# Performance work log

Hardware: AMD Instinct MI355X
Metric: run time of the kernel (lower is better)

Reference implementation:

```python
import jax, jax.numpy as jnp
import numpy as np

SEQ, D, HID, C = 512, 768, 128, 5
NENT, SPAN = 128, 16


def setup_inputs() -> dict:
    key = jax.random.key(0)
    ks = jax.random.split(key, 24)
    s = 0.02

    def rn(k, shape, scale=s):
        return jax.random.normal(k, shape, dtype=jnp.float32) * scale

    inp = {
        "encoder_output": rn(ks[0], (1, SEQ, D), 1.0),
        "holder_idxs": jax.random.randint(ks[1], (NENT, SPAN), 0, SEQ, dtype=jnp.int32),
        "target_idxs": jax.random.randint(ks[2], (NENT, SPAN), 0, SEQ, dtype=jnp.int32),
        "exp_idxs": jax.random.randint(ks[3], (NENT, SPAN), 0, SEQ, dtype=jnp.int32),
    }
    names = ["Wh_f", "bh_f", "Wh_b", "bh_b", "Wt_f", "bt_f", "Wt_b", "bt_b",
             "We_f", "be_f", "We_b", "be_b"]
    for n, k in zip(names, ks[4:16]):
        shape = (4 * HID, D) if n.startswith("W") else (4 * HID,)
        inp[n] = rn(k, shape)
    inp["T_he"] = rn(ks[16], (2 * HID, 2 * HID, 2 * HID))
    inp["T_te"] = rn(ks[17], (2 * HID, 2 * HID, 2 * HID))
    inp["T_cls"] = rn(ks[18], (2 * HID, C, 2 * HID))
    return inp


def _lstm_cell_step(x, W_ih, b):
    # Single LSTM step with h0=c0=0 (the torch module feeds seq_len=1 to nn.LSTM,
    # so W_hh @ h0 vanishes; b = b_ih + b_hh). Gate order: i, f, g, o.
    g = x @ W_ih.T + b                         # [n, L, 4H]
    i, f, gg, o = jnp.split(g, 4, axis=-1)
    c = jax.nn.sigmoid(i) * jnp.tanh(gg)
    return jax.nn.sigmoid(o) * jnp.tanh(c)     # h, [n, L, H]


def _lstm_pool(enc_seq, idxs, Wf, bf, Wb, bb):
    toks = enc_seq[idxs]                       # [n, L, D] gather
    h = jnp.concatenate([_lstm_cell_step(toks, Wf, bf),
                         _lstm_cell_step(toks, Wb, bb)], axis=-1)  # [n, L, 2H]
    return h.max(axis=1)                       # max-pool over span -> [n, 2H]


def reference(encoder_output, holder_idxs, target_idxs, exp_idxs,
              Wh_f, bh_f, Wh_b, bh_b, Wt_f, bt_f, Wt_b, bt_b,
              We_f, be_f, We_b, be_b, T_he, T_te, T_cls):
    enc = encoder_output[0]                    # [SEQ, D]
    He = _lstm_pool(enc, holder_idxs, Wh_f, bh_f, Wh_b, bh_b)   # [nh, 2H]
    Te = _lstm_pool(enc, target_idxs, Wt_f, bt_f, Wt_b, bt_b)   # [nt, 2H]
    Ee = _lstm_pool(enc, exp_idxs, We_f, be_f, We_b, be_b)      # [ne, 2H]

    # hep[i,k] = He[i] @ T_he @ Ee[k];  tep[j,k] = Te[j] @ T_te @ Ee[k]
    hep = jnp.einsum('ia,abc,kc->ikb', He, T_he, Ee)            # [nh, ne, 2H]
    tep = jnp.einsum('ja,abc,kc->jkb', Te, T_te, Ee)            # [nt, ne, 2H]
    # pred[i,j,k,m] = tep[j,k] @ T_cls[:,m,:] @ hep[i,k]
    pred = jnp.einsum('jkb,bmc,ikc->ijkm', tep, T_cls, hep)     # [nh, nt, ne, C]
    return pred
```

## Files before the change

### kernel.cpp

```cpp
#include <hip/hip_runtime.h>
#include <hip/hip_bf16.h>
#include <math.h>

#define DIM   768
#define HID   128
#define H2    256
#define NENT  128
#define SPAN  16
#define NCLS  5

#define POOLB_OFF 0
#define HEPB_OFF  196608
#define TEPB_OFF  (HEPB_OFF + 8388608)
#define TCLSB_OFF (TEPB_OFF + 8388608)
#define WB_OFF    (TCLSB_OFF + 655360)
#define TOKB_OFF  21168128
#define GATES_OFF (TOKB_OFF + 9437184)
#define PREDT_OFF 21168128

typedef __attribute__((ext_vector_type(8))) short bf16x8;
typedef __attribute__((ext_vector_type(4))) float f32x4;

__device__ __forceinline__ float sigmoidf_(float x) { return 1.0f / (1.0f + __expf(-x)); }

__device__ __forceinline__ unsigned short f2bf(float x) {
    __hip_bfloat16 h = __float2bfloat16(x);
    return *reinterpret_cast<unsigned short*>(&h);
}

__global__ __launch_bounds__(256)
void prep_kernel(const float* __restrict__ Whf, const float* __restrict__ Whb,
                 const float* __restrict__ Wtf, const float* __restrict__ Wtb,
                 const float* __restrict__ Wef, const float* __restrict__ Web,
                 const float* __restrict__ Tcls, const float* __restrict__ enc,
                 const int* __restrict__ idx_h, const int* __restrict__ idx_t,
                 const int* __restrict__ idx_e,
                 unsigned short* __restrict__ WB, unsigned short* __restrict__ TB,
                 unsigned short* __restrict__ tokB)
{
    const int bb = blockIdx.x;
    const int tid = threadIdx.x;
    if (bb < 1728) {
        int gid = bb * 256 + tid;
        int t2  = gid / 73728;
        int rem = gid % 73728;
        int n   = rem / 192;
        int c4  = rem % 192;
        int gate = n >> 7, j = n & 127;
        int srow = (gate == 0) ? j : (gate == 1) ? 256 + j : 384 + j;
        const float* W = (t2 == 0) ? Whf : (t2 == 1) ? Whb : (t2 == 2) ? Wtf :
                         (t2 == 3) ? Wtb : (t2 == 4) ? Wef : Web;
        float4 v = ((const float4*)(W + srow * DIM))[c4];
        unsigned short* d = WB + ((size_t)(t2 * 384 + n)) * DIM + c4 * 4;
        d[0] = f2bf(v.x); d[1] = f2bf(v.y); d[2] = f2bf(v.z); d[3] = f2bf(v.w);
    } else if (bb < 3008) {
        int idx = (bb - 1728) * 256 + tid;
        int b = idx / (NCLS * H2);
        int r = idx % (NCLS * H2);
        int m = r >> 8, c = r & 255;
        TB[((m << 8) + c) * H2 + b] = f2bf(Tcls[idx]);
    } else {
        int gid = (bb - 3008) * 256 + tid;
        int r  = gid / 192, c4 = gid % 192;
        int type = r >> 11;
        int rem  = r & 2047;
        const int* idx = (type == 0) ? idx_h : (type == 1) ? idx_t : idx_e;
        int row = idx[rem];
        float4 v = ((const float4*)(enc + (size_t)row * DIM))[c4];
        unsigned short h4[4] = { f2bf(v.x), f2bf(v.y), f2bf(v.z), f2bf(v.w) };
        *(uint2*)(tokB + (size_t)r * DIM + c4 * 4) = *(uint2*)h4;
    }
}

__global__ __launch_bounds__(256)
void gates_mfma(const unsigned short* __restrict__ tokB,
                const unsigned short* __restrict__ WB,
                float* __restrict__ gates)
{
    __shared__ unsigned short As[2][128 * 64];
    __shared__ unsigned short Bs[2][128 * 64];
    const int lbid = ((int)blockIdx.x & 7) * 36 + ((int)blockIdx.x >> 3);
    const int type = lbid / 96;
    const int rem  = lbid % 96;
    const int mb0  = (rem / 6) * 128;
    const int nb0  = (rem % 6) * 128;
    const int tid = threadIdx.x;
    const int w = tid >> 6, l = tid & 63;
    const int lr = l & 15, lg = l >> 4;
    const unsigned short* A = tokB + (size_t)type * 2048 * DIM + (size_t)mb0 * DIM;
    const unsigned short* B = WB   + (size_t)type * 768  * DIM + (size_t)nb0 * DIM;

    const int sr0 = tid >> 3;
    const int sc  = tid & 7;

    bf16x8 ra[4], rb[4];
    #define LOADT(kt)                                                        \
        {                                                                    \
            const int koff = (kt) * 64 + sc * 8;                             \
            _Pragma("unroll")                                                \
            for (int p = 0; p < 4; ++p) {                                    \
                int rr = sr0 + p * 32;                                       \
                ra[p] = *(const bf16x8*)(A + (size_t)rr * DIM + koff);       \
                rb[p] = *(const bf16x8*)(B + (size_t)rr * DIM + koff);       \
            }                                                                \
        }
    #define WRITET(buf)                                                      \
        {                                                                    \
            _Pragma("unroll")                                                \
            for (int p = 0; p < 4; ++p) {                                    \
                int rr = sr0 + p * 32;                                       \
                int bo = (rr * 128 + sc * 16) ^ ((rr & 7) << 4);             \
                *(bf16x8*)((char*)As[buf] + bo) = ra[p];                     \
                *(bf16x8*)((char*)Bs[buf] + bo) = rb[p];                     \
            }                                                                \
        }

    f32x4 acc[4][4];
    #pragma unroll
    for (int mt = 0; mt < 4; ++mt)
        #pragma unroll
        for (int nt = 0; nt < 4; ++nt) acc[mt][nt] = (f32x4){0.f, 0.f, 0.f, 0.f};

    const int am0 = (w & 1) * 64;
    const int bn0 = (w >> 1) * 64;

    LOADT(0);
    WRITET(0);
    __syncthreads();

    int cur = 0;
    #pragma unroll 1
    for (int kt = 0; kt < 12; ++kt) {
        if (kt + 1 < 12) LOADT(kt + 1);

        #pragma unroll
        for (int ks = 0; ks < 2; ++ks) {
            bf16x8 af[4], bf[4];
            #pragma unroll
            for (int mt = 0; mt < 4; ++mt) {
                int rr = am0 + mt * 16 + lr;
                int bo = (rr * 128 + ks * 64 + lg * 16) ^ ((rr & 7) << 4);
                af[mt] = *(const bf16x8*)((const char*)As[cur] + bo);
            }
            #pragma unroll
            for (int nt = 0; nt < 4; ++nt) {
                int rr = bn0 + nt * 16 + lr;
                int bo = (rr * 128 + ks * 64 + lg * 16) ^ ((rr & 7) << 4);
                bf[nt] = *(const bf16x8*)((const char*)Bs[cur] + bo);
            }
            #pragma unroll
            for (int mt = 0; mt < 4; ++mt)
                #pragma unroll
                for (int nt = 0; nt < 4; ++nt)
                    acc[mt][nt] = __builtin_amdgcn_mfma_f32_16x16x32_bf16(af[mt], bf[nt], acc[mt][nt], 0, 0, 0);
        }

        if (kt + 1 < 12) {
            WRITET(cur ^ 1);
        }
        __syncthreads();
        cur ^= 1;
    }
    #undef LOADT
    #undef WRITET

    float* C = gates + (size_t)type * 2048 * 768 + (size_t)mb0 * 768 + nb0;
    #pragma unroll
    for (int mt = 0; mt < 4; ++mt)
        #pragma unroll
        for (int nt = 0; nt < 4; ++nt)
            #pragma unroll
            for (int r = 0; r < 4; ++r)
                C[(size_t)(am0 + mt * 16 + lg * 4 + r) * 768 + bn0 + nt * 16 + lr] = acc[mt][nt][r];
}

__global__ __launch_bounds__(256)
void pool_epilogue(const float* __restrict__ gates,
                   const float* __restrict__ bhf, const float* __restrict__ bhb,
                   const float* __restrict__ btf, const float* __restrict__ btb,
                   const float* __restrict__ bef, const float* __restrict__ beb,
                   unsigned short* __restrict__ poolB)
{
    const int type = blockIdx.x >> 7;
    const int ent  = blockIdx.x & 127;
    const int tid  = threadIdx.x;
    const int dir  = tid >> 7;
    const int j    = tid & 127;
    const float* Bv = (type == 0) ? (dir ? bhb : bhf)
                    : (type == 1) ? (dir ? btb : btf)
                                  : (dir ? beb : bef);
    const float bi = Bv[j], bg = Bv[2 * HID + j], bo = Bv[3 * HID + j];
    const float* g0 = gates + ((size_t)type * 2048 + ent * 16) * 768 + dir * 384 + j;
    float hmax = -1e30f;
    #pragma unroll
    for (int l = 0; l < SPAN; ++l) {
        const float* gr = g0 + l * 768;
        float iv = sigmoidf_(gr[0]   + bi);
        float gv = tanhf(   gr[128] + bg);
        float ov = sigmoidf_(gr[256] + bo);
        hmax = fmaxf(hmax, ov * tanhf(iv * gv));
    }
    poolB[(size_t)(type * NENT + ent) * H2 + dir * HID + j] = f2bf(hmax);
}

__global__ __launch_bounds__(1024)
void pair_mfma(const unsigned short* __restrict__ EeB,
               const unsigned short* __restrict__ HeB,
               const unsigned short* __restrict__ TeB,
               const float* __restrict__ T0, const float* __restrict__ T1,
               unsigned short* __restrict__ hepN,
               unsigned short* __restrict__ tepN)
{
    __shared__ __align__(16) char smem[131072];
    const int bid = blockIdx.x;
    const int t = bid >> 8;
    const int b = bid & 255;
    const float* T = t ? T1 : T0;
    const unsigned short* Hx = t ? TeB : HeB;
    unsigned short* outp = t ? tepN : hepN;
    const int tid = threadIdx.x;
    const int w = tid >> 6, l = tid & 63;
    const int lr = l & 15, lg = l >> 4;

    {
        const int r0 = tid >> 5;
        const int ch = tid & 31;
        #pragma unroll
        for (int p = 0; p < 8; ++p) {
            int row = p * 32 + r0;
            const float* src = T + ((size_t)row * 256 + b) * 256 + ch * 8;
            float4 v0 = ((const float4*)src)[0];
            float4 v1 = ((const float4*)src)[1];
            bf16x8 hv; unsigned short* hp = (unsigned short*)&hv;
            hp[0]=f2bf(v0.x); hp[1]=f2bf(v0.y); hp[2]=f2bf(v0.z); hp[3]=f2bf(v0.w);
            hp[4]=f2bf(v1.x); hp[5]=f2bf(v1.y); hp[6]=f2bf(v1.z); hp[7]=f2bf(v1.w);
            int bo = (row * 512 + ch * 16) ^ ((row & 7) << 4);
            *(bf16x8*)(smem + bo) = hv;
        }
    }
    __syncthreads();

    f32x4 acc1[4][2];
    {
        const int aw = (w & 3) * 64;
        const int kw = (w >> 2) * 32;
        #pragma unroll
        for (int mt = 0; mt < 4; ++mt)
            #pragma unroll
            for (int nt = 0; nt < 2; ++nt) acc1[mt][nt] = (f32x4){0.f, 0.f, 0.f, 0.f};

        #pragma unroll
        for (int ks = 0; ks < 8; ++ks) {
            bf16x8 af[4], bf[2];
            #pragma unroll
            for (int mt = 0; mt < 4; ++mt) {
                int ar = aw + mt * 16 + lr;
                int bo = (ar * 512 + (ks * 32 + lg * 8) * 2) ^ ((ar & 7) << 4);
                af[mt] = *(const bf16x8*)(smem + bo);
            }
            #pragma unroll
            for (int nt = 0; nt < 2; ++nt)
                bf[nt] = *(const bf16x8*)(EeB + (kw + nt * 16 + lr) * H2 + ks * 32 + lg * 8);
            #pragma unroll
            for (int mt = 0; mt < 4; ++mt)
                #pragma unroll
                for (int nt = 0; nt < 2; ++nt)
                    acc1[mt][nt] = __builtin_amdgcn_mfma_f32_16x16x32_bf16(af[mt], bf[nt], acc1[mt][nt], 0, 0, 0);
        }
    }
    __syncthreads();

    {
        const int aw = (w & 3) * 64;
        const int kw = (w >> 2) * 32;
        #pragma unroll
        for (int mt = 0; mt < 4; ++mt)
            #pragma unroll
            for (int nt = 0; nt < 2; ++nt) {
                int k  = kw + nt * 16 + lr;
                int a0 = aw + mt * 16 + lg * 4;
                unsigned short h4[4] = { f2bf(acc1[mt][nt][0]), f2bf(acc1[mt][nt][1]),
                                         f2bf(acc1[mt][nt][2]), f2bf(acc1[mt][nt][3]) };
                int bo = (k * 512 + a0 * 2) ^ ((k & 7) << 4);
                *(uint2*)(smem + bo) = *(uint2*)h4;
            }
    }
    __syncthreads();

    {
        const int kw2 = (w >> 3) * 64;
        const int iw  = (w & 7) * 16;
        f32x4 acc2[4];
        #pragma unroll
        for (int mt = 0; mt < 4; ++mt) acc2[mt] = (f32x4){0.f, 0.f, 0.f, 0.f};

        #pragma unroll
        for (int ks = 0; ks < 8; ++ks) {
            bf16x8 af[4], bf;
            #pragma unroll
            for (int mt = 0; mt < 4; ++mt) {
                int kr = kw2 + mt * 16 + lr;
                int bo = (kr * 512 + (ks * 32 + lg * 8) * 2) ^ ((kr & 7) << 4);
                af[mt] = *(const bf16x8*)(smem + bo);
            }
            bf = *(const bf16x8*)(Hx + (iw + lr) * H2 + ks * 32 + lg * 8);
            #pragma unroll
            for (int mt = 0; mt < 4; ++mt)
                acc2[mt] = __builtin_amdgcn_mfma_f32_16x16x32_bf16(af[mt], bf, acc2[mt], 0, 0, 0);
        }
        unsigned short* po = outp + (size_t)b * (128 * 128);
        #pragma unroll
        for (int mt = 0; mt < 4; ++mt)
            #pragma unroll
            for (int r = 0; r < 4; ++r) {
                int k = kw2 + mt * 16 + lg * 4 + r;
                int i = iw + lr;
                po[k * 128 + i] = f2bf(acc2[mt][r]);
            }
    }
}

__global__ __launch_bounds__(512)
void step3_mfma(const unsigned short* __restrict__ hepN,
                const unsigned short* __restrict__ tepN,
                const unsigned short* __restrict__ TclsB,
                float* __restrict__ predT)
{
    __shared__ unsigned short hepS[128 * 256];
    __shared__ unsigned short tepS[64 * 256];
    __shared__ unsigned short WS[64 * 256];
    const int lbid = (blockIdx.x & 7) * 32 + (blockIdx.x >> 3);
    const int k  = lbid >> 1;
    const int jh = lbid & 1;
    const int tid = threadIdx.x;
    const int w  = tid >> 6;
    const int l  = tid & 63;
    const int lr = l & 15;
    const int lg = l >> 4;
    const int swz = (lr & 7) << 4;

    #pragma unroll
    for (int q = 0; q < 4; ++q) {
        int bcol = q * 64 + l;
        bf16x8 v = *(const bf16x8*)(tepN + ((size_t)bcol * 128 + k) * 128 + jh * 64 + w * 8);
        #pragma unroll
        for (int r = 0; r < 8; ++r) {
            int j = w * 8 + r;
            int bo = (j * 512 + bcol * 2) ^ (r << 4);
            *(unsigned short*)((char*)tepS + bo) = ((unsigned short*)&v)[r];
        }
    }
    #pragma unroll
    for (int s = 0; s < 2; ++s)
        #pragma unroll
        for (int q = 0; q < 4; ++q) {
            int bcol = q * 64 + l;
            bf16x8 v = *(const bf16x8*)(hepN + ((size_t)bcol * 128 + k) * 128 + w * 16 + s * 8);
            #pragma unroll
            for (int r = 0; r < 8; ++r) {
                int i = w * 16 + s * 8 + r;
                int bo = (i * 512 + bcol * 2) ^ (r << 4);
                *(unsigned short*)((char*)hepS + bo) = ((unsigned short*)&v)[r];
            }
        }
    __syncthreads();

    bf16x8 ha[8];
    #pragma unroll
    for (int ks = 0; ks < 8; ++ks) {
        int ir = w * 16 + lr;
        int bo = (ir * 512 + (ks * 32 + lg * 8) * 2) ^ ((ir & 7) << 4);
        ha[ks] = *(const bf16x8*)((const char*)hepS + bo);
    }

    #pragma unroll 1
    for (int m = 0; m < NCLS; ++m) {
        {
            const unsigned short* tcm = TclsB + (size_t)m * (H2 * H2);
            f32x4 acc1[4][2];
            #pragma unroll
            for (int jt = 0; jt < 4; ++jt)
                #pragma unroll
                for (int ct = 0; ct < 2; ++ct) acc1[jt][ct] = (f32x4){0.f, 0.f, 0.f, 0.f};

            #pragma unroll
            for (int ks = 0; ks < 8; ++ks) {
                bf16x8 a[4], bb[2];
                #pragma unroll
                for (int jt = 0; jt < 4; ++jt) {
                    int byteoff = ((((jt * 16 + lr) << 8) + ks * 32 + lg * 8) << 1) ^ swz;
                    a[jt] = *(const bf16x8*)((const char*)tepS + byteoff);
                }
                #pragma unroll
                for (int ct = 0; ct < 2; ++ct)
                    bb[ct] = *(const bf16x8*)(tcm + (size_t)(w * 32 + ct * 16 + lr) * H2 + ks * 32 + lg * 8);
                #pragma unroll
                for (int jt = 0; jt < 4; ++jt)
                    #pragma unroll
                    for (int ct = 0; ct < 2; ++ct)
                        acc1[jt][ct] = __builtin_amdgcn_mfma_f32_16x16x32_bf16(a[jt], bb[ct], acc1[jt][ct], 0, 0, 0);
            }
            #pragma unroll
            for (int jt = 0; jt < 4; ++jt)
                #pragma unroll
                for (int ct = 0; ct < 2; ++ct)
                    #pragma unroll
                    for (int r = 0; r < 4; ++r) {
                        int j = jt * 16 + lg * 4 + r;
                        int c = w * 32 + ct * 16 + lr;
                        int byteoff = ((((j << 8) + c)) << 1) ^ ((j & 7) << 4);
                        *(unsigned short*)((char*)WS + byteoff) = f2bf(acc1[jt][ct][r]);
                    }
        }
        __syncthreads();

        {
            f32x4 acc2[4];
            #pragma unroll
            for (int jt = 0; jt < 4; ++jt) acc2[jt] = (f32x4){0.f, 0.f, 0.f, 0.f};

            #pragma unroll
            for (int ks = 0; ks < 8; ++ks) {
                #pragma unroll
                for (int jt = 0; jt < 4; ++jt) {
                    int byteoff = ((((jt * 16 + lr) << 8) + ks * 32 + lg * 8) << 1) ^ swz;
                    bf16x8 wb = *(const bf16x8*)((const char*)WS + byteoff);
                    acc2[jt] = __builtin_amdgcn_mfma_f32_16x16x32_bf16(ha[ks], wb, acc2[jt], 0, 0, 0);
                }
            }
            float* po = predT + (size_t)(k * NCLS + m) * (NENT * NENT);
            #pragma unroll
            for (int jt = 0; jt < 4; ++jt)
                #pragma unroll
                for (int r = 0; r < 4; ++r) {
                    int i = w * 16 + lg * 4 + r;
                    int j = jh * 64 + jt * 16 + lr;
                    po[i * NENT + j] = acc2[jt][r];
                }
        }
        __syncthreads();
    }
}

__global__ __launch_bounds__(256)
void transpose_out(const float* __restrict__ predT, float* __restrict__ out)
{
    __shared__ float Ls[160][33];
    const int bid = blockIdx.x;
    const int ij0 = (bid >> 2) * 32;
    const int km0 = (bid & 3) * 160;
    const int t = threadIdx.x;

    #pragma unroll
    for (int q = 0; q < 20; ++q) {
        int r = (t >> 5) + q * 8;
        int c = t & 31;
        Ls[r][c] = predT[(size_t)(km0 + r) * 16384 + ij0 + c];
    }
    __syncthreads();
    for (int idx = t; idx < 32 * 160; idx += 256) {
        int r = idx / 160, c = idx % 160;
        out[(size_t)(ij0 + r) * 640 + km0 + c] = Ls[c][r];
    }
}

extern "C" void kernel_launch(void* const* d_in, const int* in_sizes, int n_in,
                              void* d_out, int out_size, void* d_ws, size_t ws_size,
                              hipStream_t stream)
{
    (void)in_sizes; (void)n_in; (void)out_size; (void)ws_size;
    const float* enc  = (const float*)d_in[0];
    const int*   hidx = (const int*)d_in[1];
    const int*   tidx = (const int*)d_in[2];
    const int*   eidx = (const int*)d_in[3];
    const float* Whf = (const float*)d_in[4];
    const float* bhf = (const float*)d_in[5];
    const float* Whb = (const float*)d_in[6];
    const float* bhb = (const float*)d_in[7];
    const float* Wtf = (const float*)d_in[8];
    const float* btf = (const float*)d_in[9];
    const float* Wtb = (const float*)d_in[10];
    const float* btb = (const float*)d_in[11];
    const float* Wef = (const float*)d_in[12];
    const float* bef = (const float*)d_in[13];
    const float* Web = (const float*)d_in[14];
    const float* beb = (const float*)d_in[15];
    const float* T_he  = (const float*)d_in[16];
    const float* T_te  = (const float*)d_in[17];
    const float* T_cls = (const float*)d_in[18];

    float* out = (float*)d_out;
    char*  ws  = (char*)d_ws;
    unsigned short* poolB = (unsigned short*)(ws + POOLB_OFF);
    unsigned short* hepN  = (unsigned short*)(ws + HEPB_OFF);
    unsigned short* tepN  = (unsigned short*)(ws + TEPB_OFF);
    unsigned short* TclsB = (unsigned short*)(ws + TCLSB_OFF);
    unsigned short* WB    = (unsigned short*)(ws + WB_OFF);
    unsigned short* tokB  = (unsigned short*)(ws + TOKB_OFF);
    float*          gates = (float*)(ws + GATES_OFF);
    float*          predT = (float*)(ws + PREDT_OFF);

    unsigned short* HeB = poolB;
    unsigned short* TeB = poolB + 1 * NENT * H2;
    unsigned short* EeB = poolB + 2 * NENT * H2;

    prep_kernel<<<7616, 256, 0, stream>>>(Whf, Whb, Wtf, Wtb, Wef, Web,
                                          T_cls, enc, hidx, tidx, eidx,
                                          WB, TclsB, tokB);

    gates_mfma<<<288, 256, 0, stream>>>(tokB, WB, gates);

    pool_epilogue<<<384, 256, 0, stream>>>(gates, bhf, bhb, btf, btb, bef, beb, poolB);

    pair_mfma<<<512, 1024, 0, stream>>>(EeB, HeB, TeB, T_he, T_te, hepN, tepN);

    step3_mfma<<<256, 512, 0, stream>>>(hepN, tepN, TclsB, predT);

    transpose_out<<<2048, 256, 0, stream>>>(predT, out);
}
```

Before: 134.8 us.

## Split pair bilinear into two GEMM kernels with contiguous T_he/T_te reads

Replaces the fused per-b pair kernel with two kernels. The first reads each T[a] slice contiguously and computes T[a]·Ee^T into a bf16 global intermediate laid out [b][a][k]. The second transposes each b-slice in LDS and multiplies by He/Te to produce hep/tep. This removes the strided gather over T but adds a large global round-trip for the intermediate, scalar LDS transpose stores, and an extra launch.

```diff
diff --git a/kernel.cpp b/kernel.cpp
--- a/kernel.cpp
+++ b/kernel.cpp
@@ -16,6 +16,8 @@
 #define WB_OFF    (TCLSB_OFF + 655360)
 #define TOKB_OFF  21168128
 #define GATES_OFF (TOKB_OFF + 9437184)
+#define TMP30_OFF 21168128
+#define TMP31_OFF (TMP30_OFF + 16777216)
 #define PREDT_OFF 21168128
 
 typedef __attribute__((ext_vector_type(8))) short bf16x8;
@@ -204,20 +206,16 @@
 }
 
 __global__ __launch_bounds__(1024)
-void pair_mfma(const unsigned short* __restrict__ EeB,
-               const unsigned short* __restrict__ HeB,
-               const unsigned short* __restrict__ TeB,
-               const float* __restrict__ T0, const float* __restrict__ T1,
-               unsigned short* __restrict__ hepN,
-               unsigned short* __restrict__ tepN)
+void gemm1_mfma(const unsigned short* __restrict__ EeB,
+                const float* __restrict__ T0, const float* __restrict__ T1,
+                unsigned short* __restrict__ tmp30, unsigned short* __restrict__ tmp31)
 {
     __shared__ __align__(16) char smem[131072];
     const int bid = blockIdx.x;
     const int t = bid >> 8;
-    const int b = bid & 255;
+    const int a = bid & 255;
     const float* T = t ? T1 : T0;
-    const unsigned short* Hx = t ? TeB : HeB;
-    unsigned short* outp = t ? tepN : hepN;
+    unsigned short* outp = t ? tmp31 : tmp30;
     const int tid = threadIdx.x;
     const int w = tid >> 6, l = tid & 63;
     const int lr = l & 15, lg = l >> 4;
@@ -225,10 +223,11 @@
     {
         const int r0 = tid >> 5;
         const int ch = tid & 31;
+        const float* base = T + (size_t)a * 65536;
         #pragma unroll
         for (int p = 0; p < 8; ++p) {
             int row = p * 32 + r0;
-            const float* src = T + ((size_t)row * 256 + b) * 256 + ch * 8;
+            const float* src = base + row * 256 + ch * 8;
             float4 v0 = ((const float4*)src)[0];
             float4 v1 = ((const float4*)src)[1];
             bf16x8 hv; unsigned short* hp = (unsigned short*)&hv;
@@ -240,84 +239,114 @@
     }
     __syncthreads();
 
-    f32x4 acc1[4][2];
+    const int bw = (w & 7) * 32;
+    const int kw = (w >> 3) * 64;
+    f32x4 acc[2][4];
+    #pragma unroll
+    for (int mt = 0; mt < 2; ++mt)
+        #pragma unroll
+        for (int nt = 0; nt < 4; ++nt) acc[mt][nt] = (f32x4){0.f, 0.f, 0.f, 0.f};
+
+    #pragma unroll
+    for (int ks = 0; ks < 8; ++ks) {
+        bf16x8 af[2], bf[4];
+        #pragma unroll
+        for (int mt = 0; mt < 2; ++mt) {
+            int br = bw + mt * 16 + lr;
+            int bo = (br * 512 + (ks * 32 + lg * 8) * 2) ^ ((br & 7) << 4);
+            af[mt] = *(const bf16x8*)(smem + bo);
+        }
+        #pragma unroll
+        for (int nt = 0; nt < 4; ++nt)
+            bf[nt] = *(const bf16x8*)(EeB + (kw + nt * 16 + lr) * H2 + ks * 32 + lg * 8);
+        #pragma unroll
+        for (int mt = 0; mt < 2; ++mt)
+            #pragma unroll
+            for (int nt = 0; nt < 4; ++nt)
+                acc[mt][nt] = __builtin_amdgcn_mfma_f32_16x16x32_bf16(af[mt], bf[nt], acc[mt][nt], 0, 0, 0);
+    }
+
+    #pragma unroll
+    for (int mt = 0; mt < 2; ++mt)
+        #pragma unroll
+        for (int nt = 0; nt < 4; ++nt)
+            #pragma unroll
+            for (int r = 0; r < 4; ++r) {
+                int b_ = bw + mt * 16 + lg * 4 + r;
+                int k_ = kw + nt * 16 + lr;
+                outp[((size_t)b_ * 256 + a) * 128 + k_] = f2bf(acc[mt][nt][r]);
+            }
+}
+
+__global__ __launch_bounds__(512)
+void gemm2_mfma(const unsigned short* __restrict__ HeB, const unsigned short* __restrict__ TeB,
+                const unsigned short* __restrict__ tmp30, const unsigned short* __restrict__ tmp31,
+                unsigned short* __restrict__ hepN, unsigned short* __restrict__ tepN)
+{
+    __shared__ unsigned short WT[128 * 256];
+    const int bid = blockIdx.x;
+    const int t = bid >> 8;
+    const int b = bid & 255;
+    const unsigned short* src = (t ? tmp31 : tmp30) + (size_t)b * 32768;
+    const unsigned short* Hx = t ? TeB : HeB;
+    unsigned short* outp = (t ? tepN : hepN) + (size_t)b * 16384;
+    const int tid = threadIdx.x;
+    const int w = tid >> 6, l = tid & 63;
+    const int lr = l & 15, lg = l >> 4;
+
     {
-        const int aw = (w & 3) * 64;
-        const int kw = (w >> 2) * 32;
+        const int a0 = tid >> 4;
+        const int k8 = (tid & 15) * 8;
+        #pragma unroll
+        for (int it = 0; it < 8; ++it) {
+            int aa = it * 32 + a0;
+            bf16x8 v = *(const bf16x8*)(src + aa * 128 + k8);
+            #pragma unroll
+            for (int j = 0; j < 8; ++j) {
+                int kk = k8 + j;
+                int bo = (kk * 512 + aa * 2) ^ (j << 4);
+                *(unsigned short*)((char*)WT + bo) = ((unsigned short*)&v)[j];
+            }
+        }
+    }
+    __syncthreads();
+
+    const int kw = (w & 1) * 64;
+    const int iw = (w >> 1) * 32;
+    f32x4 acc[4][2];
+    #pragma unroll
+    for (int mt = 0; mt < 4; ++mt)
+        #pragma unroll
+        for (int nt = 0; nt < 2; ++nt) acc[mt][nt] = (f32x4){0.f, 0.f, 0.f, 0.f};
+
+    #pragma unroll
+    for (int ks = 0; ks < 8; ++ks) {
+        bf16x8 af[4], bf[2];
+        #pragma unroll
+        for (int mt = 0; mt < 4; ++mt) {
+            int kr = kw + mt * 16 + lr;
+            int bo = (kr * 512 + (ks * 32 + lg * 8) * 2) ^ ((kr & 7) << 4);
+            af[mt] = *(const bf16x8*)((const char*)WT + bo);
+        }
+        #pragma unroll
+        for (int nt = 0; nt < 2; ++nt)
+            bf[nt] = *(const bf16x8*)(Hx + (iw + nt * 16 + lr) * H2 + ks * 32 + lg * 8);
         #pragma unroll
         for (int mt = 0; mt < 4; ++mt)
             #pragma unroll
-            for (int nt = 0; nt < 2; ++nt) acc1[mt][nt] = (f32x4){0.f, 0.f, 0.f, 0.f};
-
-        #pragma unroll
-        for (int ks = 0; ks < 8; ++ks) {
-            bf16x8 af[4], bf[2];
-            #pragma unroll
-            for (int mt = 0; mt < 4; ++mt) {
-                int ar = aw + mt * 16 + lr;
-                int bo = (ar * 512 + (ks * 32 + lg * 8) * 2) ^ ((ar & 7) << 4);
-                af[mt] = *(const bf16x8*)(smem + bo);
-            }
-            #pragma unroll
             for (int nt = 0; nt < 2; ++nt)
-                bf[nt] = *(const bf16x8*)(EeB + (kw + nt * 16 + lr) * H2 + ks * 32 + lg * 8);
-            #pragma unroll
-            for (int mt = 0; mt < 4; ++mt)
-                #pragma unroll
-                for (int nt = 0; nt < 2; ++nt)
-                    acc1[mt][nt] = __builtin_amdgcn_mfma_f32_16x16x32_bf16(af[mt], bf[nt], acc1[mt][nt], 0, 0, 0);
-        }
-    }
-    __syncthreads();
-
-    {
-        const int aw = (w & 3) * 64;
-        const int kw = (w >> 2) * 32;
-        #pragma unroll
-        for (int mt = 0; mt < 4; ++mt)
-            #pragma unroll
-            for (int nt = 0; nt < 2; ++nt) {
-                int k  = kw + nt * 16 + lr;
-                int a0 = aw + mt * 16 + lg * 4;
-                unsigned short h4[4] = { f2bf(acc1[mt][nt][0]), f2bf(acc1[mt][nt][1]),
-                                         f2bf(acc1[mt][nt][2]), f2bf(acc1[mt][nt][3]) };
-                int bo = (k * 512 + a0 * 2) ^ ((k & 7) << 4);
-                *(uint2*)(smem + bo) = *(uint2*)h4;
-            }
-    }
-    __syncthreads();
-
-    {
-        const int kw2 = (w >> 3) * 64;
-        const int iw  = (w & 7) * 16;
-        f32x4 acc2[4];
-        #pragma unroll
-        for (int mt = 0; mt < 4; ++mt) acc2[mt] = (f32x4){0.f, 0.f, 0.f, 0.f};
-
-        #pragma unroll
-        for (int ks = 0; ks < 8; ++ks) {
-            bf16x8 af[4], bf;
-            #pragma unroll
-            for (int mt = 0; mt < 4; ++mt) {
-                int kr = kw2 + mt * 16 + lr;
-                int bo = (kr * 512 + (ks * 32 + lg * 8) * 2) ^ ((kr & 7) << 4);
-                af[mt] = *(const bf16x8*)(smem + bo);
-            }
-            bf = *(const bf16x8*)(Hx + (iw + lr) * H2 + ks * 32 + lg * 8);
-            #pragma unroll
-            for (int mt = 0; mt < 4; ++mt)
-                acc2[mt] = __builtin_amdgcn_mfma_f32_16x16x32_bf16(af[mt], bf, acc2[mt], 0, 0, 0);
-        }
-        unsigned short* po = outp + (size_t)b * (128 * 128);
-        #pragma unroll
-        for (int mt = 0; mt < 4; ++mt)
+                acc[mt][nt] = __builtin_amdgcn_mfma_f32_16x16x32_bf16(af[mt], bf[nt], acc[mt][nt], 0, 0, 0);
+    }
+    #pragma unroll
+    for (int mt = 0; mt < 4; ++mt)
+        #pragma unroll
+        for (int nt = 0; nt < 2; ++nt)
             #pragma unroll
             for (int r = 0; r < 4; ++r) {
-                int k = kw2 + mt * 16 + lg * 4 + r;
-                int i = iw + lr;
-                po[k * 128 + i] = f2bf(acc2[mt][r]);
-            }
-    }
+                int k_ = kw + mt * 16 + lg * 4 + r;
+                int i_ = iw + nt * 16 + lr;
+                outp[k_ * 128 + i_] = f2bf(acc[mt][nt][r]);
+            }
 }
 
 __global__ __launch_bounds__(512)
@@ -498,6 +527,8 @@
     unsigned short* WB    = (unsigned short*)(ws + WB_OFF);
     unsigned short* tokB  = (unsigned short*)(ws + TOKB_OFF);
     float*          gates = (float*)(ws + GATES_OFF);
+    unsigned short* tmp30 = (unsigned short*)(ws + TMP30_OFF);
+    unsigned short* tmp31 = (unsigned short*)(ws + TMP31_OFF);
     float*          predT = (float*)(ws + PREDT_OFF);
 
     unsigned short* HeB = poolB;
@@ -512,7 +543,9 @@
 
     pool_epilogue<<<384, 256, 0, stream>>>(gates, bhf, bhb, btf, btb, bef, beb, poolB);
 
-    pair_mfma<<<512, 1024, 0, stream>>>(EeB, HeB, TeB, T_he, T_te, hepN, tepN);
+    gemm1_mfma<<<512, 1024, 0, stream>>>(EeB, T_he, T_te, tmp30, tmp31);
+
+    gemm2_mfma<<<512, 512, 0, stream>>>(HeB, TeB, tmp30, tmp31, hepN, tepN);
 
     step3_mfma<<<256, 512, 0, stream>>>(hepN, tepN, TclsB, predT);
 
```

Measured after the change: 168.5 us. 25.0% more time.

## Store gates as bf16 and pre-transpose T_he to bf16 in the pooling kernel

Applied to the files above, without the earlier changes.

The gates GEMM now writes bf16 instead of fp32, which halves gate write and read traffic. The pool epilogue kernel gains extra blocks that convert T_he to bf16 in a b-major layout, so the pair kernel's t=0 blocks read contiguous bf16 slabs instead of strided fp32 rows. The shared-memory layout in the pair kernel is reorganised into 128-byte-row banks with a new swizzle. The trade-offs are lower gate precision, since values are rounded to bf16 before the activations, and extra workspace writes for the transposed T_he.

```diff
diff --git a/kernel.cpp b/kernel.cpp
--- a/kernel.cpp
+++ b/kernel.cpp
@@ -9,14 +9,15 @@
 #define SPAN  16
 #define NCLS  5
 
-#define POOLB_OFF 0
-#define HEPB_OFF  196608
-#define TEPB_OFF  (HEPB_OFF + 8388608)
-#define TCLSB_OFF (TEPB_OFF + 8388608)
-#define WB_OFF    (TCLSB_OFF + 655360)
-#define TOKB_OFF  21168128
-#define GATES_OFF (TOKB_OFF + 9437184)
-#define PREDT_OFF 21168128
+#define POOLB_OFF  0
+#define HEPB_OFF   196608
+#define TEPB_OFF   (HEPB_OFF + 8388608)
+#define TCLSB_OFF  (TEPB_OFF + 8388608)
+#define WB_OFF     (TCLSB_OFF + 655360)
+#define TOKB_OFF   21168128
+#define TB_OFF     21168128
+#define GATESB_OFF 58060800
+#define PREDT_OFF  21168128
 
 typedef __attribute__((ext_vector_type(8))) short bf16x8;
 typedef __attribute__((ext_vector_type(4))) float f32x4;
@@ -26,6 +27,10 @@
 __device__ __forceinline__ unsigned short f2bf(float x) {
     __hip_bfloat16 h = __float2bfloat16(x);
     return *reinterpret_cast<unsigned short*>(&h);
+}
+__device__ __forceinline__ float bf2f(unsigned short u) {
+    unsigned int v = ((unsigned int)u) << 16;
+    float f; __builtin_memcpy(&f, &v, 4); return f;
 }
 
 __global__ __launch_bounds__(256)
@@ -75,7 +80,7 @@
 __global__ __launch_bounds__(256)
 void gates_mfma(const unsigned short* __restrict__ tokB,
                 const unsigned short* __restrict__ WB,
-                float* __restrict__ gates)
+                unsigned short* __restrict__ gatesB)
 {
     __shared__ unsigned short As[2][128 * 64];
     __shared__ unsigned short Bs[2][128 * 64];
@@ -164,127 +169,151 @@
     #undef LOADT
     #undef WRITET
 
-    float* C = gates + (size_t)type * 2048 * 768 + (size_t)mb0 * 768 + nb0;
+    unsigned short* C = gatesB + (size_t)type * 2048 * 768 + (size_t)mb0 * 768 + nb0;
     #pragma unroll
     for (int mt = 0; mt < 4; ++mt)
         #pragma unroll
         for (int nt = 0; nt < 4; ++nt)
             #pragma unroll
             for (int r = 0; r < 4; ++r)
-                C[(size_t)(am0 + mt * 16 + lg * 4 + r) * 768 + bn0 + nt * 16 + lr] = acc[mt][nt][r];
+                C[(size_t)(am0 + mt * 16 + lg * 4 + r) * 768 + bn0 + nt * 16 + lr] = f2bf(acc[mt][nt][r]);
 }
 
 __global__ __launch_bounds__(256)
-void pool_epilogue(const float* __restrict__ gates,
-                   const float* __restrict__ bhf, const float* __restrict__ bhb,
-                   const float* __restrict__ btf, const float* __restrict__ btb,
-                   const float* __restrict__ bef, const float* __restrict__ beb,
-                   unsigned short* __restrict__ poolB)
-{
-    const int type = blockIdx.x >> 7;
-    const int ent  = blockIdx.x & 127;
-    const int tid  = threadIdx.x;
-    const int dir  = tid >> 7;
-    const int j    = tid & 127;
-    const float* Bv = (type == 0) ? (dir ? bhb : bhf)
-                    : (type == 1) ? (dir ? btb : btf)
-                                  : (dir ? beb : bef);
-    const float bi = Bv[j], bg = Bv[2 * HID + j], bo = Bv[3 * HID + j];
-    const float* g0 = gates + ((size_t)type * 2048 + ent * 16) * 768 + dir * 384 + j;
-    float hmax = -1e30f;
-    #pragma unroll
-    for (int l = 0; l < SPAN; ++l) {
-        const float* gr = g0 + l * 768;
-        float iv = sigmoidf_(gr[0]   + bi);
-        float gv = tanhf(   gr[128] + bg);
-        float ov = sigmoidf_(gr[256] + bo);
-        hmax = fmaxf(hmax, ov * tanhf(iv * gv));
-    }
-    poolB[(size_t)(type * NENT + ent) * H2 + dir * HID + j] = f2bf(hmax);
+void poolconv(const unsigned short* __restrict__ gatesB,
+              const float* __restrict__ bhf, const float* __restrict__ bhb,
+              const float* __restrict__ btf, const float* __restrict__ btb,
+              const float* __restrict__ bef, const float* __restrict__ beb,
+              unsigned short* __restrict__ poolB,
+              const float* __restrict__ T0, unsigned short* __restrict__ TB)
+{
+    const int bb = blockIdx.x;
+    const int tid = threadIdx.x;
+    if (bb < 384) {
+        const int type = bb >> 7;
+        const int ent  = bb & 127;
+        const int dir  = tid >> 7;
+        const int j    = tid & 127;
+        const float* Bv = (type == 0) ? (dir ? bhb : bhf)
+                        : (type == 1) ? (dir ? btb : btf)
+                                      : (dir ? beb : bef);
+        const float bi = Bv[j], bg = Bv[2 * HID + j], bo = Bv[3 * HID + j];
+        const unsigned short* g0 = gatesB + ((size_t)type * 2048 + ent * 16) * 768 + dir * 384 + j;
+        float hmax = -1e30f;
+        #pragma unroll
+        for (int ll = 0; ll < SPAN; ++ll) {
+            const unsigned short* gr = g0 + ll * 768;
+            float iv = sigmoidf_(bf2f(gr[0])   + bi);
+            float gv = tanhf(   bf2f(gr[128]) + bg);
+            float ov = sigmoidf_(bf2f(gr[256]) + bo);
+            hmax = fmaxf(hmax, ov * tanhf(iv * gv));
+        }
+        poolB[(size_t)(type * NENT + ent) * H2 + dir * HID + j] = f2bf(hmax);
+    } else {
+        int W0 = (bb - 384) * 256 + tid;
+        #pragma unroll 1
+        for (int it = 0; it < 16; ++it) {
+            int idx = W0 + it * 131072;
+            int a  = idx >> 13;
+            int rr = idx & 8191;
+            int b  = rr >> 5;
+            int c8 = rr & 31;
+            const float* src = T0 + ((size_t)(a * 256 + b) << 8) + c8 * 8;
+            float4 v0 = ((const float4*)src)[0];
+            float4 v1 = ((const float4*)src)[1];
+            bf16x8 hv; unsigned short* hp = (unsigned short*)&hv;
+            hp[0]=f2bf(v0.x); hp[1]=f2bf(v0.y); hp[2]=f2bf(v0.z); hp[3]=f2bf(v0.w);
+            hp[4]=f2bf(v1.x); hp[5]=f2bf(v1.y); hp[6]=f2bf(v1.z); hp[7]=f2bf(v1.w);
+            *(bf16x8*)(TB + (((size_t)(b * 256 + a)) << 8) + c8 * 8) = hv;
+        }
+    }
 }
 
 __global__ __launch_bounds__(1024)
-void pair_mfma(const unsigned short* __restrict__ EeB,
-               const unsigned short* __restrict__ HeB,
-               const unsigned short* __restrict__ TeB,
-               const float* __restrict__ T0, const float* __restrict__ T1,
-               unsigned short* __restrict__ hepN,
-               unsigned short* __restrict__ tepN)
+void pairc_mfma(const unsigned short* __restrict__ EeB,
+                const unsigned short* __restrict__ HeB,
+                const unsigned short* __restrict__ TeB,
+                const unsigned short* __restrict__ TB,
+                const float* __restrict__ T1,
+                unsigned short* __restrict__ hepN, unsigned short* __restrict__ tepN)
 {
     __shared__ __align__(16) char smem[131072];
     const int bid = blockIdx.x;
     const int t = bid >> 8;
     const int b = bid & 255;
-    const float* T = t ? T1 : T0;
     const unsigned short* Hx = t ? TeB : HeB;
     unsigned short* outp = t ? tepN : hepN;
     const int tid = threadIdx.x;
     const int w = tid >> 6, l = tid & 63;
     const int lr = l & 15, lg = l >> 4;
 
-    {
-        const int r0 = tid >> 5;
-        const int ch = tid & 31;
+    if (t == 0) {
+        const unsigned short* TBb = TB + (size_t)b * 65536;
         #pragma unroll
         for (int p = 0; p < 8; ++p) {
-            int row = p * 32 + r0;
-            const float* src = T + ((size_t)row * 256 + b) * 256 + ch * 8;
+            int L = tid + p * 1024;
+            int row = L >> 5, ch = L & 31;
+            bf16x8 v = *(const bf16x8*)(TBb + (size_t)L * 8);
+            int bo = (((ch >> 3) << 15) + row * 128 + ((ch & 7) << 4)) ^ ((row & 7) << 4);
+            *(bf16x8*)(smem + bo) = v;
+        }
+    } else {
+        #pragma unroll
+        for (int p = 0; p < 8; ++p) {
+            int L = tid + p * 1024;
+            int row = L >> 5, ch = L & 31;
+            const float* src = T1 + ((size_t)row * 256 + b) * 256 + ch * 8;
             float4 v0 = ((const float4*)src)[0];
             float4 v1 = ((const float4*)src)[1];
             bf16x8 hv; unsigned short* hp = (unsigned short*)&hv;
             hp[0]=f2bf(v0.x); hp[1]=f2bf(v0.y); hp[2]=f2bf(v0.z); hp[3]=f2bf(v0.w);
             hp[4]=f2bf(v1.x); hp[5]=f2bf(v1.y); hp[6]=f2bf(v1.z); hp[7]=f2bf(v1.w);
-            int bo = (row * 512 + ch * 16) ^ ((row & 7) << 4);
+            int bo = (((ch >> 3) << 15) + row * 128 + ((ch & 7) << 4)) ^ ((row & 7) << 4);
             *(bf16x8*)(smem + bo) = hv;
         }
     }
     __syncthreads();
 
     f32x4 acc1[4][2];
-    {
-        const int aw = (w & 3) * 64;
-        const int kw = (w >> 2) * 32;
+    const int aw = (w & 3) * 64;
+    const int kw = (w >> 2) * 32;
+    #pragma unroll
+    for (int mt = 0; mt < 4; ++mt)
+        #pragma unroll
+        for (int nt = 0; nt < 2; ++nt) acc1[mt][nt] = (f32x4){0.f, 0.f, 0.f, 0.f};
+
+    #pragma unroll
+    for (int ks = 0; ks < 8; ++ks) {
+        const int cb = ks * 64 + lg * 16;
+        bf16x8 af[4], bf[2];
+        #pragma unroll
+        for (int mt = 0; mt < 4; ++mt) {
+            int a = aw + mt * 16 + lr;
+            int bo = (((cb >> 7) << 15) + a * 128 + (cb & 127)) ^ ((a & 7) << 4);
+            af[mt] = *(const bf16x8*)(smem + bo);
+        }
+        #pragma unroll
+        for (int nt = 0; nt < 2; ++nt)
+            bf[nt] = *(const bf16x8*)(EeB + (kw + nt * 16 + lr) * H2 + ks * 32 + lg * 8);
         #pragma unroll
         for (int mt = 0; mt < 4; ++mt)
             #pragma unroll
-            for (int nt = 0; nt < 2; ++nt) acc1[mt][nt] = (f32x4){0.f, 0.f, 0.f, 0.f};
-
-        #pragma unroll
-        for (int ks = 0; ks < 8; ++ks) {
-            bf16x8 af[4], bf[2];
-            #pragma unroll
-            for (int mt = 0; mt < 4; ++mt) {
-                int ar = aw + mt * 16 + lr;
-                int bo = (ar * 512 + (ks * 32 + lg * 8) * 2) ^ ((ar & 7) << 4);
-                af[mt] = *(const bf16x8*)(smem + bo);
-            }
-            #pragma unroll
             for (int nt = 0; nt < 2; ++nt)
-                bf[nt] = *(const bf16x8*)(EeB + (kw + nt * 16 + lr) * H2 + ks * 32 + lg * 8);
-            #pragma unroll
-            for (int mt = 0; mt < 4; ++mt)
-                #pragma unroll
-                for (int nt = 0; nt < 2; ++nt)
-                    acc1[mt][nt] = __builtin_amdgcn_mfma_f32_16x16x32_bf16(af[mt], bf[nt], acc1[mt][nt], 0, 0, 0);
-        }
+                acc1[mt][nt] = __builtin_amdgcn_mfma_f32_16x16x32_bf16(af[mt], bf[nt], acc1[mt][nt], 0, 0, 0);
     }
     __syncthreads();
 
-    {
-        const int aw = (w & 3) * 64;
-        const int kw = (w >> 2) * 32;
-        #pragma unroll
-        for (int mt = 0; mt < 4; ++mt)
-            #pragma unroll
-            for (int nt = 0; nt < 2; ++nt) {
-                int k  = kw + nt * 16 + lr;
-                int a0 = aw + mt * 16 + lg * 4;
-                unsigned short h4[4] = { f2bf(acc1[mt][nt][0]), f2bf(acc1[mt][nt][1]),
-                                         f2bf(acc1[mt][nt][2]), f2bf(acc1[mt][nt][3]) };
-                int bo = (k * 512 + a0 * 2) ^ ((k & 7) << 4);
-                *(uint2*)(smem + bo) = *(uint2*)h4;
-            }
-    }
+    #pragma unroll
+    for (int mt = 0; mt < 4; ++mt)
+        #pragma unroll
+        for (int nt = 0; nt < 2; ++nt) {
+            int k  = kw + nt * 16 + lr;
+            int a0 = aw + mt * 16 + lg * 4;
+            unsigned short h4[4] = { f2bf(acc1[mt][nt][0]), f2bf(acc1[mt][nt][1]),
+                                     f2bf(acc1[mt][nt][2]), f2bf(acc1[mt][nt][3]) };
+            int bo = (((a0 >> 6) << 14) + k * 128 + ((a0 & 63) << 1)) ^ ((k & 7) << 4);
+            *(uint2*)(smem + bo) = *(uint2*)h4;
+        }
     __syncthreads();
 
     {
@@ -296,11 +325,12 @@
 
         #pragma unroll
         for (int ks = 0; ks < 8; ++ks) {
+            const int ab = ks * 64 + lg * 16;
             bf16x8 af[4], bf;
             #pragma unroll
             for (int mt = 0; mt < 4; ++mt) {
-                int kr = kw2 + mt * 16 + lr;
-                int bo = (kr * 512 + (ks * 32 + lg * 8) * 2) ^ ((kr & 7) << 4);
+                int k = kw2 + mt * 16 + lr;
+                int bo = (((ab >> 7) << 14) + k * 128 + (ab & 127)) ^ ((k & 7) << 4);
                 af[mt] = *(const bf16x8*)(smem + bo);
             }
             bf = *(const bf16x8*)(Hx + (iw + lr) * H2 + ks * 32 + lg * 8);
@@ -491,14 +521,15 @@
 
     float* out = (float*)d_out;
     char*  ws  = (char*)d_ws;
-    unsigned short* poolB = (unsigned short*)(ws + POOLB_OFF);
-    unsigned short* hepN  = (unsigned short*)(ws + HEPB_OFF);
-    unsigned short* tepN  = (unsigned short*)(ws + TEPB_OFF);
-    unsigned short* TclsB = (unsigned short*)(ws + TCLSB_OFF);
-    unsigned short* WB    = (unsigned short*)(ws + WB_OFF);
-    unsigned short* tokB  = (unsigned short*)(ws + TOKB_OFF);
-    float*          gates = (float*)(ws + GATES_OFF);
-    float*          predT = (float*)(ws + PREDT_OFF);
+    unsigned short* poolB  = (unsigned short*)(ws + POOLB_OFF);
+    unsigned short* hepN   = (unsigned short*)(ws + HEPB_OFF);
+    unsigned short* tepN   = (unsigned short*)(ws + TEPB_OFF);
+    unsigned short* TclsB  = (unsigned short*)(ws + TCLSB_OFF);
+    unsigned short* WB     = (unsigned short*)(ws + WB_OFF);
+    unsigned short* tokB   = (unsigned short*)(ws + TOKB_OFF);
+    unsigned short* TB     = (unsigned short*)(ws + TB_OFF);
+    unsigned short* gatesB = (unsigned short*)(ws + GATESB_OFF);
+    float*          predT  = (float*)(ws + PREDT_OFF);
 
     unsigned short* HeB = poolB;
     unsigned short* TeB = poolB + 1 * NENT * H2;
@@ -508,11 +539,12 @@
                                           T_cls, enc, hidx, tidx, eidx,
                                           WB, TclsB, tokB);
 
-    gates_mfma<<<288, 256, 0, stream>>>(tokB, WB, gates);
-
-    pool_epilogue<<<384, 256, 0, stream>>>(gates, bhf, bhb, btf, btb, bef, beb, poolB);
-
-    pair_mfma<<<512, 1024, 0, stream>>>(EeB, HeB, TeB, T_he, T_te, hepN, tepN);
+    gates_mfma<<<288, 256, 0, stream>>>(tokB, WB, gatesB);
+
+    poolconv<<<896, 256, 0, stream>>>(gatesB, bhf, bhb, btf, btb, bef, beb,
+                                      poolB, T_he, TB);
+
+    pairc_mfma<<<512, 1024, 0, stream>>>(EeB, HeB, TeB, TB, T_te, hepN, tepN);
 
     step3_mfma<<<256, 512, 0, stream>>>(hepN, tepN, TclsB, predT);
 
```

New measurement: 140.9 us. 1.04x slower.

## Store gates in bf16, pre-transpose hep/tep, split step3 into finer blocks

Applied to the files above, without the earlier changes.

The gates GEMM now writes bf16 instead of fp32, which halves the gates traffic between gates_mfma and pool_epilogue. A new transpose kernel rewrites hep/tep into a k-major layout so step3 can load contiguous rows instead of doing a scattered transposing gather. step3 is split into 512 blocks, each covering 32 j values, to use more CUs with smaller LDS. This adds one kernel launch and an extra round trip through memory for the transpose, rounds the gate pre-activations to bf16, and makes each block recompute the hep fragments.

```diff
diff --git a/kernel.cpp b/kernel.cpp
--- a/kernel.cpp
+++ b/kernel.cpp
@@ -9,14 +9,16 @@
 #define SPAN  16
 #define NCLS  5
 
-#define POOLB_OFF 0
-#define HEPB_OFF  196608
-#define TEPB_OFF  (HEPB_OFF + 8388608)
-#define TCLSB_OFF (TEPB_OFF + 8388608)
-#define WB_OFF    (TCLSB_OFF + 655360)
-#define TOKB_OFF  21168128
-#define GATES_OFF (TOKB_OFF + 9437184)
-#define PREDT_OFF 21168128
+#define POOLB_OFF  0
+#define TCLSB_OFF  196608
+#define HEPT_OFF   851968
+#define TEPT_OFF   9240576
+#define HEPN_OFF   17629184
+#define TEPN_OFF   26017792
+#define GATESB_OFF 17629184
+#define PREDT_OFF  17629184
+#define WB_OFF     59572224
+#define TOKB_OFF   63111168
 
 typedef __attribute__((ext_vector_type(8))) short bf16x8;
 typedef __attribute__((ext_vector_type(4))) float f32x4;
@@ -26,6 +28,10 @@
 __device__ __forceinline__ unsigned short f2bf(float x) {
     __hip_bfloat16 h = __float2bfloat16(x);
     return *reinterpret_cast<unsigned short*>(&h);
+}
+__device__ __forceinline__ float bf2f(unsigned short u) {
+    unsigned int v = ((unsigned int)u) << 16;
+    float f; __builtin_memcpy(&f, &v, 4); return f;
 }
 
 __global__ __launch_bounds__(256)
@@ -75,7 +81,7 @@
 __global__ __launch_bounds__(256)
 void gates_mfma(const unsigned short* __restrict__ tokB,
                 const unsigned short* __restrict__ WB,
-                float* __restrict__ gates)
+                unsigned short* __restrict__ gatesB)
 {
     __shared__ unsigned short As[2][128 * 64];
     __shared__ unsigned short Bs[2][128 * 64];
@@ -164,18 +170,18 @@
     #undef LOADT
     #undef WRITET
 
-    float* C = gates + (size_t)type * 2048 * 768 + (size_t)mb0 * 768 + nb0;
+    unsigned short* C = gatesB + (size_t)type * 2048 * 768 + (size_t)mb0 * 768 + nb0;
     #pragma unroll
     for (int mt = 0; mt < 4; ++mt)
         #pragma unroll
         for (int nt = 0; nt < 4; ++nt)
             #pragma unroll
             for (int r = 0; r < 4; ++r)
-                C[(size_t)(am0 + mt * 16 + lg * 4 + r) * 768 + bn0 + nt * 16 + lr] = acc[mt][nt][r];
+                C[(size_t)(am0 + mt * 16 + lg * 4 + r) * 768 + bn0 + nt * 16 + lr] = f2bf(acc[mt][nt][r]);
 }
 
 __global__ __launch_bounds__(256)
-void pool_epilogue(const float* __restrict__ gates,
+void pool_epilogue(const unsigned short* __restrict__ gatesB,
                    const float* __restrict__ bhf, const float* __restrict__ bhb,
                    const float* __restrict__ btf, const float* __restrict__ btb,
                    const float* __restrict__ bef, const float* __restrict__ beb,
@@ -190,14 +196,14 @@
                     : (type == 1) ? (dir ? btb : btf)
                                   : (dir ? beb : bef);
     const float bi = Bv[j], bg = Bv[2 * HID + j], bo = Bv[3 * HID + j];
-    const float* g0 = gates + ((size_t)type * 2048 + ent * 16) * 768 + dir * 384 + j;
+    const unsigned short* g0 = gatesB + ((size_t)type * 2048 + ent * 16) * 768 + dir * 384 + j;
     float hmax = -1e30f;
     #pragma unroll
-    for (int l = 0; l < SPAN; ++l) {
-        const float* gr = g0 + l * 768;
-        float iv = sigmoidf_(gr[0]   + bi);
-        float gv = tanhf(   gr[128] + bg);
-        float ov = sigmoidf_(gr[256] + bo);
+    for (int ll = 0; ll < SPAN; ++ll) {
+        const unsigned short* gr = g0 + ll * 768;
+        float iv = sigmoidf_(bf2f(gr[0])   + bi);
+        float gv = tanhf(   bf2f(gr[128]) + bg);
+        float ov = sigmoidf_(bf2f(gr[256]) + bo);
         hmax = fmaxf(hmax, ov * tanhf(iv * gv));
     }
     poolB[(size_t)(type * NENT + ent) * H2 + dir * HID + j] = f2bf(hmax);
@@ -320,122 +326,135 @@
     }
 }
 
+__global__ __launch_bounds__(256)
+void trT(const unsigned short* __restrict__ hepN, const unsigned short* __restrict__ tepN,
+         unsigned short* __restrict__ hepT, unsigned short* __restrict__ tepT)
+{
+    __shared__ unsigned short L[128 * 256];
+    const int t = blockIdx.x >> 7;
+    const int k = blockIdx.x & 127;
+    const unsigned short* src = t ? tepN : hepN;
+    unsigned short* dst = (t ? tepT : hepT) + (size_t)k * 32768;
+    const int tid = threadIdx.x;
+
+    #pragma unroll
+    for (int it = 0; it < 16; ++it) {
+        int g = it * 256 + tid;
+        int b = g >> 4, i8 = g & 15;
+        bf16x8 v = *(const bf16x8*)(src + (size_t)b * 16384 + k * 128 + i8 * 8);
+        #pragma unroll
+        for (int e = 0; e < 8; ++e) {
+            int i = i8 * 8 + e;
+            int bo = (i * 512 + b * 2) ^ ((i8 & 7) << 4);
+            *(unsigned short*)((char*)L + bo) = ((unsigned short*)&v)[e];
+        }
+    }
+    __syncthreads();
+
+    #pragma unroll
+    for (int it = 0; it < 16; ++it) {
+        int h = it * 256 + tid;
+        int i = h >> 5, ch = h & 31;
+        int bo = (i * 512 + ch * 16) ^ (((i >> 3) & 7) << 4);
+        bf16x8 v = *(const bf16x8*)((const char*)L + bo);
+        *(bf16x8*)(dst + i * 256 + ch * 8) = v;
+    }
+}
+
 __global__ __launch_bounds__(512)
-void step3_mfma(const unsigned short* __restrict__ hepN,
-                const unsigned short* __restrict__ tepN,
-                const unsigned short* __restrict__ TclsB,
-                float* __restrict__ predT)
-{
-    __shared__ unsigned short hepS[128 * 256];
-    __shared__ unsigned short tepS[64 * 256];
-    __shared__ unsigned short WS[64 * 256];
-    const int lbid = (blockIdx.x & 7) * 32 + (blockIdx.x >> 3);
-    const int k  = lbid >> 1;
-    const int jh = lbid & 1;
+void step3v2(const unsigned short* __restrict__ hepT,
+             const unsigned short* __restrict__ tepT,
+             const unsigned short* __restrict__ TclsB,
+             float* __restrict__ predT)
+{
+    __shared__ unsigned short tepS[32 * 256];
+    __shared__ unsigned short WS[32 * 256];
+    const int lbid = ((int)blockIdx.x & 7) * 64 + ((int)blockIdx.x >> 3);
+    const int k  = lbid >> 2;
+    const int jq = lbid & 3;
+    const int j0 = jq * 32;
     const int tid = threadIdx.x;
-    const int w  = tid >> 6;
-    const int l  = tid & 63;
-    const int lr = l & 15;
-    const int lg = l >> 4;
-    const int swz = (lr & 7) << 4;
-
-    #pragma unroll
-    for (int q = 0; q < 4; ++q) {
-        int bcol = q * 64 + l;
-        bf16x8 v = *(const bf16x8*)(tepN + ((size_t)bcol * 128 + k) * 128 + jh * 64 + w * 8);
-        #pragma unroll
-        for (int r = 0; r < 8; ++r) {
-            int j = w * 8 + r;
-            int bo = (j * 512 + bcol * 2) ^ (r << 4);
-            *(unsigned short*)((char*)tepS + bo) = ((unsigned short*)&v)[r];
-        }
-    }
-    #pragma unroll
-    for (int s = 0; s < 2; ++s)
-        #pragma unroll
-        for (int q = 0; q < 4; ++q) {
-            int bcol = q * 64 + l;
-            bf16x8 v = *(const bf16x8*)(hepN + ((size_t)bcol * 128 + k) * 128 + w * 16 + s * 8);
-            #pragma unroll
-            for (int r = 0; r < 8; ++r) {
-                int i = w * 16 + s * 8 + r;
-                int bo = (i * 512 + bcol * 2) ^ (r << 4);
-                *(unsigned short*)((char*)hepS + bo) = ((unsigned short*)&v)[r];
-            }
-        }
-    __syncthreads();
+    const int w = tid >> 6, l = tid & 63;
+    const int lr = l & 15, lg = l >> 4;
+
+    #pragma unroll
+    for (int it = 0; it < 2; ++it) {
+        int g = it * 512 + tid;
+        int row = g >> 5, ch = g & 31;
+        bf16x8 v = *(const bf16x8*)(tepT + ((size_t)k * 128 + j0 + row) * 256 + ch * 8);
+        int bo = (row * 512 + ch * 16) ^ ((row & 7) << 4);
+        *(bf16x8*)((char*)tepS + bo) = v;
+    }
 
     bf16x8 ha[8];
     #pragma unroll
-    for (int ks = 0; ks < 8; ++ks) {
-        int ir = w * 16 + lr;
-        int bo = (ir * 512 + (ks * 32 + lg * 8) * 2) ^ ((ir & 7) << 4);
-        ha[ks] = *(const bf16x8*)((const char*)hepS + bo);
-    }
+    for (int ks = 0; ks < 8; ++ks)
+        ha[ks] = *(const bf16x8*)(hepT + ((size_t)k * 128 + w * 16 + lr) * 256 + ks * 32 + lg * 8);
+    __syncthreads();
 
     #pragma unroll 1
     for (int m = 0; m < NCLS; ++m) {
         {
             const unsigned short* tcm = TclsB + (size_t)m * (H2 * H2);
-            f32x4 acc1[4][2];
-            #pragma unroll
-            for (int jt = 0; jt < 4; ++jt)
-                #pragma unroll
-                for (int ct = 0; ct < 2; ++ct) acc1[jt][ct] = (f32x4){0.f, 0.f, 0.f, 0.f};
+            f32x4 a1[2][2];
+            #pragma unroll
+            for (int jt = 0; jt < 2; ++jt)
+                #pragma unroll
+                for (int ct = 0; ct < 2; ++ct) a1[jt][ct] = (f32x4){0.f, 0.f, 0.f, 0.f};
 
             #pragma unroll
             for (int ks = 0; ks < 8; ++ks) {
-                bf16x8 a[4], bb[2];
-                #pragma unroll
-                for (int jt = 0; jt < 4; ++jt) {
-                    int byteoff = ((((jt * 16 + lr) << 8) + ks * 32 + lg * 8) << 1) ^ swz;
-                    a[jt] = *(const bf16x8*)((const char*)tepS + byteoff);
+                bf16x8 a[2], bb[2];
+                #pragma unroll
+                for (int jt = 0; jt < 2; ++jt) {
+                    int bo = ((jt * 16 + lr) * 512 + (ks * 32 + lg * 8) * 2) ^ ((lr & 7) << 4);
+                    a[jt] = *(const bf16x8*)((const char*)tepS + bo);
                 }
                 #pragma unroll
                 for (int ct = 0; ct < 2; ++ct)
                     bb[ct] = *(const bf16x8*)(tcm + (size_t)(w * 32 + ct * 16 + lr) * H2 + ks * 32 + lg * 8);
                 #pragma unroll
-                for (int jt = 0; jt < 4; ++jt)
+                for (int jt = 0; jt < 2; ++jt)
                     #pragma unroll
                     for (int ct = 0; ct < 2; ++ct)
-                        acc1[jt][ct] = __builtin_amdgcn_mfma_f32_16x16x32_bf16(a[jt], bb[ct], acc1[jt][ct], 0, 0, 0);
-            }
-            #pragma unroll
-            for (int jt = 0; jt < 4; ++jt)
+                        a1[jt][ct] = __builtin_amdgcn_mfma_f32_16x16x32_bf16(a[jt], bb[ct], a1[jt][ct], 0, 0, 0);
+            }
+            #pragma unroll
+            for (int jt = 0; jt < 2; ++jt)
                 #pragma unroll
                 for (int ct = 0; ct < 2; ++ct)
                     #pragma unroll
                     for (int r = 0; r < 4; ++r) {
                         int j = jt * 16 + lg * 4 + r;
                         int c = w * 32 + ct * 16 + lr;
-                        int byteoff = ((((j << 8) + c)) << 1) ^ ((j & 7) << 4);
-                        *(unsigned short*)((char*)WS + byteoff) = f2bf(acc1[jt][ct][r]);
+                        int bo = (j * 512 + c * 2) ^ ((j & 7) << 4);
+                        *(unsigned short*)((char*)WS + bo) = f2bf(a1[jt][ct][r]);
                     }
         }
         __syncthreads();
 
         {
-            f32x4 acc2[4];
-            #pragma unroll
-            for (int jt = 0; jt < 4; ++jt) acc2[jt] = (f32x4){0.f, 0.f, 0.f, 0.f};
+            f32x4 a2[2];
+            #pragma unroll
+            for (int jt = 0; jt < 2; ++jt) a2[jt] = (f32x4){0.f, 0.f, 0.f, 0.f};
 
             #pragma unroll
             for (int ks = 0; ks < 8; ++ks) {
                 #pragma unroll
-                for (int jt = 0; jt < 4; ++jt) {
-                    int byteoff = ((((jt * 16 + lr) << 8) + ks * 32 + lg * 8) << 1) ^ swz;
-                    bf16x8 wb = *(const bf16x8*)((const char*)WS + byteoff);
-                    acc2[jt] = __builtin_amdgcn_mfma_f32_16x16x32_bf16(ha[ks], wb, acc2[jt], 0, 0, 0);
+                for (int jt = 0; jt < 2; ++jt) {
+                    int bo = ((jt * 16 + lr) * 512 + (ks * 32 + lg * 8) * 2) ^ ((lr & 7) << 4);
+                    bf16x8 wb = *(const bf16x8*)((const char*)WS + bo);
+                    a2[jt] = __builtin_amdgcn_mfma_f32_16x16x32_bf16(ha[ks], wb, a2[jt], 0, 0, 0);
                 }
             }
             float* po = predT + (size_t)(k * NCLS + m) * (NENT * NENT);
             #pragma unroll
-            for (int jt = 0; jt < 4; ++jt)
+            for (int jt = 0; jt < 2; ++jt)
                 #pragma unroll
                 for (int r = 0; r < 4; ++r) {
                     int i = w * 16 + lg * 4 + r;
-                    int j = jh * 64 + jt * 16 + lr;
-                    po[i * NENT + j] = acc2[jt][r];
+                    int j = j0 + jt * 16 + lr;
+                    po[i * NENT + j] = a2[jt][r];
                 }
         }
         __syncthreads();
@@ -491,14 +510,16 @@
 
     float* out = (float*)d_out;
     char*  ws  = (char*)d_ws;
-    unsigned short* poolB = (unsigned short*)(ws + POOLB_OFF);
-    unsigned short* hepN  = (unsigned short*)(ws + HEPB_OFF);
-    unsigned short* tepN  = (unsigned short*)(ws + TEPB_OFF);
-    unsigned short* TclsB = (unsigned short*)(ws + TCLSB_OFF);
-    unsigned short* WB    = (unsigned short*)(ws + WB_OFF);
-    unsigned short* tokB  = (unsigned short*)(ws + TOKB_OFF);
-    float*          gates = (float*)(ws + GATES_OFF);
-    float*          predT = (float*)(ws + PREDT_OFF);
+    unsigned short* poolB  = (unsigned short*)(ws + POOLB_OFF);
+    unsigned short* TclsB  = (unsigned short*)(ws + TCLSB_OFF);
+    unsigned short* hepT   = (unsigned short*)(ws + HEPT_OFF);
+    unsigned short* tepT   = (unsigned short*)(ws + TEPT_OFF);
+    unsigned short* hepN   = (unsigned short*)(ws + HEPN_OFF);
+    unsigned short* tepN   = (unsigned short*)(ws + TEPN_OFF);
+    unsigned short* gatesB = (unsigned short*)(ws + GATESB_OFF);
+    float*          predT  = (float*)(ws + PREDT_OFF);
+    unsigned short* WB     = (unsigned short*)(ws + WB_OFF);
+    unsigned short* tokB   = (unsigned short*)(ws + TOKB_OFF);
 
     unsigned short* HeB = poolB;
     unsigned short* TeB = poolB + 1 * NENT * H2;
@@ -508,13 +529,15 @@
                                           T_cls, enc, hidx, tidx, eidx,
                                           WB, TclsB, tokB);
 
-    gates_mfma<<<288, 256, 0, stream>>>(tokB, WB, gates);
-
-    pool_epilogue<<<384, 256, 0, stream>>>(gates, bhf, bhb, btf, btb, bef, beb, poolB);
+    gates_mfma<<<288, 256, 0, stream>>>(tokB, WB, gatesB);
+
+    pool_epilogue<<<384, 256, 0, stream>>>(gatesB, bhf, bhb, btf, btb, bef, beb, poolB);
 
     pair_mfma<<<512, 1024, 0, stream>>>(EeB, HeB, TeB, T_he, T_te, hepN, tepN);
 
-    step3_mfma<<<256, 512, 0, stream>>>(hepN, tepN, TclsB, predT);
+    trT<<<256, 256, 0, stream>>>(hepN, tepN, hepT, tepT);
+
+    step3v2<<<512, 512, 0, stream>>>(hepT, tepT, TclsB, predT);
 
     transpose_out<<<2048, 256, 0, stream>>>(predT, out);
 }
```

Measured after the change: 152.6 us. +13.1%, slower.
